# Kernel optimization log

Hardware: AMD Instinct MI355X
Metric: run time of the kernel (lower is better)

The kernel has to match this reference:

```python
import jax, jax.numpy as jnp
import numpy as np

H = 16  # num_heads

def setup_inputs() -> dict:
    key = jax.random.key(0)
    k1, k2, k3, k4 = jax.random.split(key, 4)
    B, N, E = 2, 2048, 2048
    return {
        "hidden_states": jax.random.normal(k1, (B, N, E), jnp.float32),
        "w_fused": jax.random.normal(k2, (E, 3 * E), jnp.float32) * (E ** -0.5),
        "w_proj": jax.random.normal(k3, (E, E), jnp.float32) * (E ** -0.5),
        "b_proj": jax.random.normal(k4, (E,), jnp.float32),
    }

def reference(hidden_states, w_fused, w_proj, b_proj):
    B, N, E = hidden_states.shape
    D = E // H  # head_dim
    qkv = hidden_states @ w_fused                      # [B,N,3E]
    q, k, v = jnp.split(qkv, 3, axis=-1)               # each [B,N,E]
    def to_heads(t):
        return t.reshape(B, N, H, D).transpose(0, 2, 1, 3)  # [B,H,N,D]
    q, k, v = to_heads(q), to_heads(k), to_heads(v)
    scores = jnp.einsum('bhnd,bhmd->bhnm', q, k) / jnp.asarray(D ** 0.5, q.dtype)
    causal = jnp.tril(jnp.ones((N, N), dtype=bool))    # [N,N]
    mask_value = jnp.asarray(jnp.finfo(scores.dtype).min, scores.dtype)
    scores = jnp.where(causal[None, None], scores, mask_value)
    attn_weights = jax.nn.softmax(scores, axis=-1)     # [B,H,N,N]
    attn_out = jnp.einsum('bhnm,bhmd->bhnd', attn_weights, v)
    attn_out = attn_out.transpose(0, 2, 1, 3).reshape(B, N, E)  # b n (h d)
    out = attn_out @ w_proj + b_proj
    return out, attn_weights
```

## Files before the change

### kernel.cpp

```cpp
#include <hip/hip_runtime.h>
#include <hip/hip_bf16.h>

typedef __attribute__((ext_vector_type(4))) float f32x4;
typedef __attribute__((ext_vector_type(8))) __bf16 bf16x8;


__device__ inline unsigned short f2bf(float f) {
  union { float f; unsigned u; } x; x.f = f;
  unsigned r = x.u + 0x7fffu + ((x.u >> 16) & 1u);
  return (unsigned short)(r >> 16);
}

__device__ inline void stage_bf16_tile(const ushort* __restrict__ g, int ldg, ushort* l) {
  int tid = threadIdx.x;
#pragma unroll
  for (int t = 0; t < 4; ++t) {
    int c = tid + t * 256;
    int m = c >> 3, kc = (c & 7) << 3;
    *(int4*)(l + m * 72 + kc) = *(const int4*)(g + (size_t)m * ldg + kc);
  }
}

__device__ inline void mma_tile(const ushort* lA, const ushort* lB, f32x4 acc[4][4]) {
  int lane = threadIdx.x & 63, w = threadIdx.x >> 6;
  int wm = (w & 1) << 6, wn = (w >> 1) << 6;
  int row = lane & 15, quad = lane >> 4;
#pragma unroll
  for (int kk = 0; kk < 64; kk += 32) {
    bf16x8 a[4], b[4];
#pragma unroll
    for (int i = 0; i < 4; ++i)
      a[i] = *(const bf16x8*)(lA + (wm + i * 16 + row) * 72 + kk + quad * 8);
#pragma unroll
    for (int j = 0; j < 4; ++j)
      b[j] = *(const bf16x8*)(lB + (wn + j * 16 + row) * 72 + kk + quad * 8);
#pragma unroll
    for (int i = 0; i < 4; ++i)
#pragma unroll
      for (int j = 0; j < 4; ++j)
        acc[i][j] = __builtin_amdgcn_mfma_f32_16x16x32_bf16(a[i], b[j], acc[i][j], 0, 0, 0);
  }
}

__device__ inline void mma_pv(const ushort* lP, const ushort* lV, int kk2, f32x4 acc[4][4]) {
  int lane = threadIdx.x & 63, w = threadIdx.x >> 6;
  int wm = (w & 1) << 6, wn = (w >> 1) << 6;
  int row = lane & 15, quad = lane >> 4;
#pragma unroll
  for (int kk = 0; kk < 64; kk += 32) {
    bf16x8 a[4], b[4];
#pragma unroll
    for (int i = 0; i < 4; ++i)
      a[i] = *(const bf16x8*)(lP + (wm + i * 16 + row) * 136 + kk2 * 64 + kk + quad * 8);
#pragma unroll
    for (int j = 0; j < 4; ++j)
      b[j] = *(const bf16x8*)(lV + (wn + j * 16 + row) * 72 + kk + quad * 8);
#pragma unroll
    for (int i = 0; i < 4; ++i)
#pragma unroll
      for (int j = 0; j < 4; ++j)
        acc[i][j] = __builtin_amdgcn_mfma_f32_16x16x32_bf16(a[i], b[j], acc[i][j], 0, 0, 0);
  }
}


__global__ __launch_bounds__(256) void k_cvt_bf16(const float* __restrict__ in,
                                                  ushort* __restrict__ out, int n4) {
  int i = blockIdx.x * 256 + threadIdx.x;
  if (i >= n4) return;
  float4 v = *(const float4*)(in + (size_t)i * 4);
  ushort4 o; o.x = f2bf(v.x); o.y = f2bf(v.y); o.z = f2bf(v.z); o.w = f2bf(v.w);
  *(ushort4*)(out + (size_t)i * 4) = o;
}

__global__ __launch_bounds__(256) void k_transpose_bf16(const float* __restrict__ in,
                                                        ushort* __restrict__ out, int R, int C) {
  __shared__ __align__(16) ushort t[64][72];
  int c0 = blockIdx.x << 6, r0 = blockIdx.y << 6;
  int tid = threadIdx.x;
#pragma unroll
  for (int it = 0; it < 4; ++it) {
    int idx = tid + it * 256;
    int r = idx >> 4, c4 = (idx & 15) << 2;
    float4 v = *(const float4*)(in + (size_t)(r0 + r) * C + c0 + c4);
    t[c4][r] = f2bf(v.x); t[c4 + 1][r] = f2bf(v.y);
    t[c4 + 2][r] = f2bf(v.z); t[c4 + 3][r] = f2bf(v.w);
  }
  __syncthreads();
#pragma unroll
  for (int it = 0; it < 4; ++it) {
    int idx = tid + it * 256;
    int c = idx >> 4, r4 = (idx & 15) << 2;
    ushort4 o; o.x = t[c][r4]; o.y = t[c][r4 + 1]; o.z = t[c][r4 + 2]; o.w = t[c][r4 + 3];
    *(ushort4*)(out + (size_t)(c0 + c) * R + r0 + r4) = o;
  }
}

__global__ __launch_bounds__(256) void k_qkv(const ushort* __restrict__ A,
                                             const ushort* __restrict__ Bt,
                                             ushort* __restrict__ qh,
                                             ushort* __restrict__ kh,
                                             ushort* __restrict__ vt) {
  __shared__ __align__(16) ushort lA[128 * 72];
  __shared__ __align__(16) ushort lB[128 * 72];
  int rt = blockIdx.x, ct = blockIdx.y;
  f32x4 z = {0.f, 0.f, 0.f, 0.f};
  f32x4 acc[4][4];
#pragma unroll
  for (int i = 0; i < 4; ++i)
#pragma unroll
    for (int j = 0; j < 4; ++j) acc[i][j] = z;
  for (int kt = 0; kt < 2048; kt += 64) {
    __syncthreads();
    stage_bf16_tile(A + (size_t)rt * 128 * 2048 + kt, 2048, lA);
    stage_bf16_tile(Bt + (size_t)ct * 128 * 2048 + kt, 2048, lB);
    __syncthreads();
    mma_tile(lA, lB, acc);
  }
  int lane = threadIdx.x & 63, w = threadIdx.x >> 6;
  int wm = (w & 1) << 6, wn = (w >> 1) << 6;
  int col = lane & 15, rb = (lane >> 4) << 2;
#pragma unroll
  for (int i = 0; i < 4; ++i)
#pragma unroll
    for (int j = 0; j < 4; ++j)
#pragma unroll
      for (int r = 0; r < 4; ++r) {
        int R = rt * 128 + wm + i * 16 + rb + r;
        int C = ct * 128 + wn + j * 16 + col;
        int b = R >> 11, n = R & 2047;
        int seg = C >> 11, hh = (C >> 7) & 15, d = C & 127;
        int bh = b * 16 + hh;
        float v = acc[i][j][r];
        if (seg == 0)      qh[((size_t)bh * 2048 + n) * 128 + d] = f2bf(v * 0.08838834764831845f);
        else if (seg == 1) kh[((size_t)bh * 2048 + n) * 128 + d] = f2bf(v);
        else               vt[((size_t)bh * 128 + d) * 2048 + n] = f2bf(v);
      }
}

__global__ __launch_bounds__(256, 2) void k_attn(const ushort* __restrict__ qh,
                                                 const ushort* __restrict__ kh,
                                                 const ushort* __restrict__ vt,
                                                 float* __restrict__ attnw,
                                                 ushort* __restrict__ Ao) {
  __shared__ __align__(16) ushort lAB[2 * 128 * 72];
  __shared__ __align__(16) ushort lV[128 * 72];
  __shared__ float mArr[128], lArr[128], invA[128], tm0[128], tm1[128];

  int id = blockIdx.x;
  int r5 = id & 31, p = r5 >> 1;
  int rt = (r5 & 1) ? p : 15 - p;
  int bh = ((id >> 5) << 1) | ((id >> 4) & 1);

  ushort* lA = lAB;
  ushort* lB = lAB + 128 * 72;
  int tid = threadIdx.x;
  int lane = tid & 63, w = tid >> 6;
  int wm = (w & 1) << 6, wn = (w >> 1) << 6;
  int c16 = lane & 15, quad = lane >> 4;

  const ushort* Qb = qh + ((size_t)bh * 2048 + rt * 128) * 128;
  const ushort* Kb = kh + (size_t)bh * 2048 * 128;
  const ushort* Vb = vt + (size_t)bh * 128 * 2048;
  float* Pg = attnw + (size_t)bh * 2048 * 2048 + (size_t)rt * 128 * 2048;

  if (tid < 128) { mArr[tid] = -INFINITY; lArr[tid] = 0.f; }
  __syncthreads();

  f32x4 z = {0.f, 0.f, 0.f, 0.f};
  float* tmw = (wn == 0) ? tm0 : tm1;

  for (int ct = 0; ct <= rt; ++ct) {
    f32x4 acc[4][4];
#pragma unroll
    for (int i = 0; i < 4; ++i)
#pragma unroll
      for (int j = 0; j < 4; ++j) acc[i][j] = z;
#pragma unroll
    for (int kt = 0; kt < 128; kt += 64) {
      __syncthreads();
      stage_bf16_tile(Qb + kt, 128, lA);
      stage_bf16_tile(Kb + (size_t)ct * 128 * 128 + kt, 128, lB);
      __syncthreads();
      mma_tile(lA, lB, acc);
    }
    bool diag = (ct == rt);
#pragma unroll
    for (int i = 0; i < 4; ++i)
#pragma unroll
      for (int r = 0; r < 4; ++r) {
        int lr = wm + i * 16 + quad * 4 + r;
        float mx = -INFINITY;
#pragma unroll
        for (int j = 0; j < 4; ++j) {
          int lc = wn + j * 16 + c16;
          if (!diag || lc <= lr) mx = fmaxf(mx, acc[i][j][r]);
        }
#pragma unroll
        for (int o = 1; o < 16; o <<= 1) mx = fmaxf(mx, __shfl_xor(mx, o));
        if (c16 == 0) tmw[lr] = mx;
      }
    __syncthreads();
    if (tid < 128) {
      float tmax = fmaxf(tm0[tid], tm1[tid]);
      float mo = mArr[tid];
      float mn = fmaxf(mo, tmax);
      float corr = (mo == -INFINITY) ? 0.f : __expf(mo - mn);
      mArr[tid] = mn;
      lArr[tid] *= corr;
    }
    __syncthreads();
#pragma unroll
    for (int i = 0; i < 4; ++i)
#pragma unroll
      for (int r = 0; r < 4; ++r) {
        int lr = wm + i * 16 + quad * 4 + r;
        float mn = mArr[lr];
        float s = 0.f;
#pragma unroll
        for (int j = 0; j < 4; ++j) {
          int lc = wn + j * 16 + c16;
          if (!diag || lc <= lr) s += __expf(acc[i][j][r] - mn);
        }
#pragma unroll
        for (int o = 1; o < 16; o <<= 1) s += __shfl_xor(s, o);
        if (c16 == 0) tmw[lr] = s;
      }
    __syncthreads();
    if (tid < 128) lArr[tid] += tm0[tid] + tm1[tid];
  }
  __syncthreads();
  if (tid < 128) invA[tid] = 1.f / lArr[tid];
  __syncthreads();

  f32x4 o2[4][4];
#pragma unroll
  for (int i = 0; i < 4; ++i)
#pragma unroll
    for (int j = 0; j < 4; ++j) o2[i][j] = z;

  for (int ct = 0; ct <= rt; ++ct) {
    f32x4 acc[4][4];
#pragma unroll
    for (int i = 0; i < 4; ++i)
#pragma unroll
      for (int j = 0; j < 4; ++j) acc[i][j] = z;
#pragma unroll
    for (int kt = 0; kt < 128; kt += 64) {
      __syncthreads();
      stage_bf16_tile(Qb + kt, 128, lA);
      stage_bf16_tile(Kb + (size_t)ct * 128 * 128 + kt, 128, lB);
      __syncthreads();
      mma_tile(lA, lB, acc);
    }
    __syncthreads();
    bool diag = (ct == rt);
    ushort* lP = lAB;
#pragma unroll
    for (int i = 0; i < 4; ++i)
#pragma unroll
      for (int r = 0; r < 4; ++r) {
        int lr = wm + i * 16 + quad * 4 + r;
        float mn = mArr[lr], inv = invA[lr];
        float* prow = Pg + (size_t)lr * 2048 + ct * 128;
#pragma unroll
        for (int j = 0; j < 4; ++j) {
          int lc = wn + j * 16 + c16;
          float e = (!diag || lc <= lr) ? __expf(acc[i][j][r] - mn) * inv : 0.f;
          lP[lr * 136 + lc] = f2bf(e);
          prow[lc] = e;
        }
      }
    stage_bf16_tile(Vb + ct * 128, 2048, lV);
    __syncthreads();
    mma_pv(lP, lV, 0, o2);
    __syncthreads();
    stage_bf16_tile(Vb + ct * 128 + 64, 2048, lV);
    __syncthreads();
    mma_pv(lP, lV, 1, o2);
  }

  float4 z4 = make_float4(0.f, 0.f, 0.f, 0.f);
  for (int ct = rt + 1; ct < 16; ++ct) {
    float* T = Pg + ct * 128;
#pragma unroll
    for (int it = 0; it < 16; ++it) {
      int idx = tid + it * 256;
      int rr = idx >> 5, cc = (idx & 31) << 2;
      *(float4*)(T + (size_t)rr * 2048 + cc) = z4;
    }
  }

  int b = bh >> 4, hh = bh & 15;
#pragma unroll
  for (int i = 0; i < 4; ++i)
#pragma unroll
    for (int j = 0; j < 4; ++j)
#pragma unroll
      for (int r = 0; r < 4; ++r) {
        int R = rt * 128 + wm + i * 16 + quad * 4 + r;
        int C = wn + j * 16 + c16;
        Ao[((size_t)b * 2048 + R) * 2048 + hh * 128 + C] = f2bf(o2[i][j][r]);
      }
}

__global__ __launch_bounds__(256) void k_proj(const ushort* __restrict__ Ao,
                                              const ushort* __restrict__ Wt,
                                              const float* __restrict__ bias,
                                              float* __restrict__ out) {
  int rt = blockIdx.x, ct = blockIdx.y;
  __shared__ __align__(16) ushort lA[128 * 72];
  __shared__ __align__(16) ushort lB[128 * 72];
  f32x4 z = {0.f, 0.f, 0.f, 0.f};
  f32x4 acc[4][4];
#pragma unroll
  for (int i = 0; i < 4; ++i)
#pragma unroll
    for (int j = 0; j < 4; ++j) acc[i][j] = z;
  for (int kt = 0; kt < 2048; kt += 64) {
    __syncthreads();
    stage_bf16_tile(Ao + (size_t)rt * 128 * 2048 + kt, 2048, lA);
    stage_bf16_tile(Wt + (size_t)ct * 128 * 2048 + kt, 2048, lB);
    __syncthreads();
    mma_tile(lA, lB, acc);
  }
  int lane = threadIdx.x & 63, w = threadIdx.x >> 6;
  int wm = (w & 1) << 6, wn = (w >> 1) << 6;
  int col = lane & 15, rb = (lane >> 4) << 2;
#pragma unroll
  for (int i = 0; i < 4; ++i)
#pragma unroll
    for (int j = 0; j < 4; ++j)
#pragma unroll
      for (int r = 0; r < 4; ++r) {
        int R = rt * 128 + wm + i * 16 + rb + r;
        int C = ct * 128 + wn + j * 16 + col;
        out[(size_t)R * 2048 + C] = acc[i][j][r] + bias[C];
      }
}


extern "C" void kernel_launch(void* const* d_in, const int* in_sizes, int n_in,
                              void* d_out, int out_size, void* d_ws, size_t ws_size,
                              hipStream_t stream) {
  const float* hs = (const float*)d_in[0];
  const float* wf = (const float*)d_in[1];
  const float* wp = (const float*)d_in[2];
  const float* bp = (const float*)d_in[3];
  float* out = (float*)d_out;
  float* attnw = out + (size_t)8388608;

  ushort* Hb  = (ushort*)d_ws;
  ushort* Wft = Hb  + (size_t)8388608;
  ushort* Wpt = Wft + (size_t)12582912;
  ushort* qh  = Wpt + (size_t)4194304;
  ushort* kh  = qh  + (size_t)8388608;
  ushort* vt  = kh  + (size_t)8388608;
  ushort* Ao  = vt  + (size_t)8388608;

  k_cvt_bf16<<<8192, 256, 0, stream>>>(hs, Hb, 2097152);
  k_transpose_bf16<<<dim3(96, 32), 256, 0, stream>>>(wf, Wft, 2048, 6144);
  k_transpose_bf16<<<dim3(32, 32), 256, 0, stream>>>(wp, Wpt, 2048, 2048);
  k_qkv<<<dim3(32, 48), 256, 0, stream>>>(Hb, Wft, qh, kh, vt);
  k_attn<<<512, 256, 0, stream>>>(qh, kh, vt, attnw, Ao);
  k_proj<<<dim3(32, 16), 256, 0, stream>>>(Ao, Wpt, bp, out);
}
```

Baseline: 1.129 ms.

## Single-pass online-softmax attention with direct-to-LDS loads and fixup kernel for weights

Attention moves from a two-pass scheme (one pass for max/sum, a second that recomputes QK and does PV) to a single online-softmax pass. Raw scores are written to the attention-weights buffer and later normalised by a separate fixup kernel that also writes the causal zeros. Q is kept in registers, and K/V tiles are staged through XOR-swizzled LDS using global_load_lds. The same swizzled direct-to-LDS staging replaces padded shared tiles in the QKV and projection GEMMs, and attention blocks are remapped for locality. The cost is an extra read and write pass over the large attention-weights tensor in exchange for dropping the QK recompute and part of the LDS traffic.

```diff
diff --git a/kernel.cpp b/kernel.cpp
--- a/kernel.cpp
+++ b/kernel.cpp
@@ -11,50 +11,47 @@
   return (unsigned short)(r >> 16);
 }
 
-__device__ inline void stage_bf16_tile(const ushort* __restrict__ g, int ldg, ushort* l) {
+__device__ inline void gload16(const ushort* g, ushort* l) {
+  __builtin_amdgcn_global_load_lds(
+      (const __attribute__((address_space(1))) unsigned int*)(const void*)g,
+      (__attribute__((address_space(3))) unsigned int*)(void*)l, 16, 0, 0);
+}
+
+__device__ inline void stage64(const ushort* __restrict__ g, int ldg, ushort* l) {
   int tid = threadIdx.x;
 #pragma unroll
   for (int t = 0; t < 4; ++t) {
     int c = tid + t * 256;
-    int m = c >> 3, kc = (c & 7) << 3;
-    *(int4*)(l + m * 72 + kc) = *(const int4*)(g + (size_t)m * ldg + kc);
-  }
-}
-
-__device__ inline void mma_tile(const ushort* lA, const ushort* lB, f32x4 acc[4][4]) {
+    int m = c >> 3, q = (c & 7) ^ (m & 7);
+    gload16(g + (size_t)m * ldg + q * 8, l + c * 8);
+  }
+}
+
+__device__ inline void stage128(const ushort* __restrict__ g, int ldg, ushort* l) {
+  int tid = threadIdx.x;
+#pragma unroll
+  for (int t = 0; t < 8; ++t) {
+    int c = tid + t * 256;
+    int m = c >> 4, q = (c & 15) ^ (m & 15);
+    gload16(g + (size_t)m * ldg + q * 8, l + c * 8);
+  }
+}
+
+__device__ inline void mma_tile64(const ushort* lA, const ushort* lB, f32x4 acc[4][4]) {
   int lane = threadIdx.x & 63, w = threadIdx.x >> 6;
   int wm = (w & 1) << 6, wn = (w >> 1) << 6;
   int row = lane & 15, quad = lane >> 4;
+  int r7 = row & 7;
 #pragma unroll
   for (int kk = 0; kk < 64; kk += 32) {
+    int sw = (((kk >> 3) + quad) ^ r7) << 3;
     bf16x8 a[4], b[4];
 #pragma unroll
     for (int i = 0; i < 4; ++i)
-      a[i] = *(const bf16x8*)(lA + (wm + i * 16 + row) * 72 + kk + quad * 8);
+      a[i] = *(const bf16x8*)(lA + (wm + i * 16 + row) * 64 + sw);
 #pragma unroll
     for (int j = 0; j < 4; ++j)
-      b[j] = *(const bf16x8*)(lB + (wn + j * 16 + row) * 72 + kk + quad * 8);
-#pragma unroll
-    for (int i = 0; i < 4; ++i)
-#pragma unroll
-      for (int j = 0; j < 4; ++j)
-        acc[i][j] = __builtin_amdgcn_mfma_f32_16x16x32_bf16(a[i], b[j], acc[i][j], 0, 0, 0);
-  }
-}
-
-__device__ inline void mma_pv(const ushort* lP, const ushort* lV, int kk2, f32x4 acc[4][4]) {
-  int lane = threadIdx.x & 63, w = threadIdx.x >> 6;
-  int wm = (w & 1) << 6, wn = (w >> 1) << 6;
-  int row = lane & 15, quad = lane >> 4;
-#pragma unroll
-  for (int kk = 0; kk < 64; kk += 32) {
-    bf16x8 a[4], b[4];
-#pragma unroll
-    for (int i = 0; i < 4; ++i)
-      a[i] = *(const bf16x8*)(lP + (wm + i * 16 + row) * 136 + kk2 * 64 + kk + quad * 8);
-#pragma unroll
-    for (int j = 0; j < 4; ++j)
-      b[j] = *(const bf16x8*)(lV + (wn + j * 16 + row) * 72 + kk + quad * 8);
+      b[j] = *(const bf16x8*)(lB + (wn + j * 16 + row) * 64 + sw);
 #pragma unroll
     for (int i = 0; i < 4; ++i)
 #pragma unroll
@@ -101,8 +98,8 @@
                                              ushort* __restrict__ qh,
                                              ushort* __restrict__ kh,
                                              ushort* __restrict__ vt) {
-  __shared__ __align__(16) ushort lA[128 * 72];
-  __shared__ __align__(16) ushort lB[128 * 72];
+  __shared__ __align__(16) ushort lA[128 * 64];
+  __shared__ __align__(16) ushort lB[128 * 64];
   int rt = blockIdx.x, ct = blockIdx.y;
   f32x4 z = {0.f, 0.f, 0.f, 0.f};
   f32x4 acc[4][4];
@@ -112,10 +109,10 @@
     for (int j = 0; j < 4; ++j) acc[i][j] = z;
   for (int kt = 0; kt < 2048; kt += 64) {
     __syncthreads();
-    stage_bf16_tile(A + (size_t)rt * 128 * 2048 + kt, 2048, lA);
-    stage_bf16_tile(Bt + (size_t)ct * 128 * 2048 + kt, 2048, lB);
-    __syncthreads();
-    mma_tile(lA, lB, acc);
+    stage64(A + (size_t)rt * 128 * 2048 + kt, 2048, lA);
+    stage64(Bt + (size_t)ct * 128 * 2048 + kt, 2048, lB);
+    __syncthreads();
+    mma_tile64(lA, lB, acc);
   }
   int lane = threadIdx.x & 63, w = threadIdx.x >> 6;
   int wm = (w & 1) << 6, wn = (w >> 1) << 6;
@@ -142,18 +139,19 @@
                                                  const ushort* __restrict__ kh,
                                                  const ushort* __restrict__ vt,
                                                  float* __restrict__ attnw,
-                                                 ushort* __restrict__ Ao) {
-  __shared__ __align__(16) ushort lAB[2 * 128 * 72];
-  __shared__ __align__(16) ushort lV[128 * 72];
-  __shared__ float mArr[128], lArr[128], invA[128], tm0[128], tm1[128];
-
-  int id = blockIdx.x;
+                                                 ushort* __restrict__ Ao,
+                                                 float* __restrict__ mf,
+                                                 float* __restrict__ il) {
+  __shared__ __align__(16) ushort lKP[128 * 128];
+  __shared__ __align__(16) ushort lV[128 * 128];
+  __shared__ float mArr[128], lArr[128], corrArr[128], invA[128], tm0[128], tm1[128];
+
+  int raw = blockIdx.x;
+  int id = (raw & 7) * 64 + (raw >> 3);
   int r5 = id & 31, p = r5 >> 1;
   int rt = (r5 & 1) ? p : 15 - p;
   int bh = ((id >> 5) << 1) | ((id >> 4) & 1);
 
-  ushort* lA = lAB;
-  ushort* lB = lAB + 128 * 72;
   int tid = threadIdx.x;
   int lane = tid & 63, w = tid >> 6;
   int wm = (w & 1) << 6, wn = (w >> 1) << 6;
@@ -164,26 +162,48 @@
   const ushort* Vb = vt + (size_t)bh * 128 * 2048;
   float* Pg = attnw + (size_t)bh * 2048 * 2048 + (size_t)rt * 128 * 2048;
 
+  bf16x8 q[4][4];
+#pragma unroll
+  for (int i = 0; i < 4; ++i)
+#pragma unroll
+    for (int ks = 0; ks < 4; ++ks)
+      q[i][ks] = *(const bf16x8*)(Qb + (size_t)(wm + i * 16 + c16) * 128 + ks * 32 + quad * 8);
+
   if (tid < 128) { mArr[tid] = -INFINITY; lArr[tid] = 0.f; }
-  __syncthreads();
 
   f32x4 z = {0.f, 0.f, 0.f, 0.f};
+  f32x4 o2[4][4];
+#pragma unroll
+  for (int i = 0; i < 4; ++i)
+#pragma unroll
+    for (int j = 0; j < 4; ++j) o2[i][j] = z;
   float* tmw = (wn == 0) ? tm0 : tm1;
 
   for (int ct = 0; ct <= rt; ++ct) {
+    __syncthreads();
+    stage128(Kb + (size_t)ct * 128 * 128, 128, lKP);
+    __syncthreads();
+    stage128(Vb + ct * 128, 2048, lV);
+
     f32x4 acc[4][4];
 #pragma unroll
     for (int i = 0; i < 4; ++i)
 #pragma unroll
       for (int j = 0; j < 4; ++j) acc[i][j] = z;
 #pragma unroll
-    for (int kt = 0; kt < 128; kt += 64) {
-      __syncthreads();
-      stage_bf16_tile(Qb + kt, 128, lA);
-      stage_bf16_tile(Kb + (size_t)ct * 128 * 128 + kt, 128, lB);
-      __syncthreads();
-      mma_tile(lA, lB, acc);
+    for (int ks = 0; ks < 4; ++ks) {
+      int sw = (((ks << 2) + quad) ^ c16) << 3;
+      bf16x8 b[4];
+#pragma unroll
+      for (int j = 0; j < 4; ++j)
+        b[j] = *(const bf16x8*)(lKP + (wn + j * 16 + c16) * 128 + sw);
+#pragma unroll
+      for (int i = 0; i < 4; ++i)
+#pragma unroll
+        for (int j = 0; j < 4; ++j)
+          acc[i][j] = __builtin_amdgcn_mfma_f32_16x16x32_bf16(q[i][ks], b[j], acc[i][j], 0, 0, 0);
     }
+
     bool diag = (ct == rt);
 #pragma unroll
     for (int i = 0; i < 4; ++i)
@@ -206,21 +226,27 @@
       float mo = mArr[tid];
       float mn = fmaxf(mo, tmax);
       float corr = (mo == -INFINITY) ? 0.f : __expf(mo - mn);
-      mArr[tid] = mn;
-      lArr[tid] *= corr;
+      mArr[tid] = mn; corrArr[tid] = corr; lArr[tid] *= corr;
     }
     __syncthreads();
+
 #pragma unroll
     for (int i = 0; i < 4; ++i)
 #pragma unroll
       for (int r = 0; r < 4; ++r) {
         int lr = wm + i * 16 + quad * 4 + r;
-        float mn = mArr[lr];
+        float mn = mArr[lr], corr = corrArr[lr];
         float s = 0.f;
+        float* prow = Pg + (size_t)lr * 2048 + ct * 128;
 #pragma unroll
         for (int j = 0; j < 4; ++j) {
           int lc = wn + j * 16 + c16;
-          if (!diag || lc <= lr) s += __expf(acc[i][j][r] - mn);
+          float sv = acc[i][j][r];
+          prow[lc] = sv;
+          float e = (!diag || lc <= lr) ? __expf(sv - mn) : 0.f;
+          s += e;
+          lKP[lr * 128 + ((((lc >> 3) ^ (lr & 15)) << 3) | (lc & 7))] = f2bf(e);
+          o2[i][j][r] *= corr;
         }
 #pragma unroll
         for (int o = 1; o < 16; o <<= 1) s += __shfl_xor(s, o);
@@ -228,80 +254,73 @@
       }
     __syncthreads();
     if (tid < 128) lArr[tid] += tm0[tid] + tm1[tid];
+
+#pragma unroll
+    for (int ks = 0; ks < 4; ++ks) {
+      int sw = (((ks << 2) + quad) ^ c16) << 3;
+      bf16x8 a[4], b[4];
+#pragma unroll
+      for (int i = 0; i < 4; ++i)
+        a[i] = *(const bf16x8*)(lKP + (wm + i * 16 + c16) * 128 + sw);
+#pragma unroll
+      for (int j = 0; j < 4; ++j)
+        b[j] = *(const bf16x8*)(lV + (wn + j * 16 + c16) * 128 + sw);
+#pragma unroll
+      for (int i = 0; i < 4; ++i)
+#pragma unroll
+        for (int j = 0; j < 4; ++j)
+          o2[i][j] = __builtin_amdgcn_mfma_f32_16x16x32_bf16(a[i], b[j], o2[i][j], 0, 0, 0);
+    }
+  }
+
+  if (tid < 128) {
+    float iv = 1.f / lArr[tid];
+    invA[tid] = iv;
+    int g = bh * 2048 + rt * 128 + tid;
+    mf[g] = mArr[tid]; il[g] = iv;
   }
   __syncthreads();
-  if (tid < 128) invA[tid] = 1.f / lArr[tid];
-  __syncthreads();
-
-  f32x4 o2[4][4];
-#pragma unroll
-  for (int i = 0; i < 4; ++i)
-#pragma unroll
-    for (int j = 0; j < 4; ++j) o2[i][j] = z;
-
-  for (int ct = 0; ct <= rt; ++ct) {
-    f32x4 acc[4][4];
-#pragma unroll
-    for (int i = 0; i < 4; ++i)
-#pragma unroll
-      for (int j = 0; j < 4; ++j) acc[i][j] = z;
-#pragma unroll
-    for (int kt = 0; kt < 128; kt += 64) {
-      __syncthreads();
-      stage_bf16_tile(Qb + kt, 128, lA);
-      stage_bf16_tile(Kb + (size_t)ct * 128 * 128 + kt, 128, lB);
-      __syncthreads();
-      mma_tile(lA, lB, acc);
+  int b = bh >> 4, hh = bh & 15;
+#pragma unroll
+  for (int i = 0; i < 4; ++i)
+#pragma unroll
+    for (int j = 0; j < 4; ++j)
+#pragma unroll
+      for (int r = 0; r < 4; ++r) {
+        int lr = wm + i * 16 + quad * 4 + r;
+        int R = rt * 128 + lr;
+        int C = wn + j * 16 + c16;
+        Ao[((size_t)b * 2048 + R) * 2048 + hh * 128 + C] = f2bf(o2[i][j][r] * invA[lr]);
+      }
+}
+
+__global__ __launch_bounds__(256) void k_fixup(float* __restrict__ attnw,
+                                               const float* __restrict__ mf,
+                                               const float* __restrict__ il) {
+  int n = blockIdx.x, bh = blockIdx.y;
+  float m = mf[bh * 2048 + n];
+  float inv = il[bh * 2048 + n];
+  float* row = attnw + ((size_t)bh * 2048 + n) * 2048;
+  int tid = threadIdx.x;
+#pragma unroll
+  for (int t = 0; t < 2; ++t) {
+    int c0 = (tid + t * 256) << 2;
+    float4 o;
+    if (c0 + 3 <= n) {
+      float4 s = *(const float4*)(row + c0);
+      o.x = __expf(s.x - m) * inv; o.y = __expf(s.y - m) * inv;
+      o.z = __expf(s.z - m) * inv; o.w = __expf(s.w - m) * inv;
+    } else if (c0 > n) {
+      o = make_float4(0.f, 0.f, 0.f, 0.f);
+    } else {
+      float4 s = *(const float4*)(row + c0);
+      o.x = (c0     <= n) ? __expf(s.x - m) * inv : 0.f;
+      o.y = (c0 + 1 <= n) ? __expf(s.y - m) * inv : 0.f;
+      o.z = (c0 + 2 <= n) ? __expf(s.z - m) * inv : 0.f;
+      o.w = (c0 + 3 <= n) ? __expf(s.w - m) * inv : 0.f;
     }
-    __syncthreads();
-    bool diag = (ct == rt);
-    ushort* lP = lAB;
-#pragma unroll
-    for (int i = 0; i < 4; ++i)
-#pragma unroll
-      for (int r = 0; r < 4; ++r) {
-        int lr = wm + i * 16 + quad * 4 + r;
-        float mn = mArr[lr], inv = invA[lr];
-        float* prow = Pg + (size_t)lr * 2048 + ct * 128;
-#pragma unroll
-        for (int j = 0; j < 4; ++j) {
-          int lc = wn + j * 16 + c16;
-          float e = (!diag || lc <= lr) ? __expf(acc[i][j][r] - mn) * inv : 0.f;
-          lP[lr * 136 + lc] = f2bf(e);
-          prow[lc] = e;
-        }
-      }
-    stage_bf16_tile(Vb + ct * 128, 2048, lV);
-    __syncthreads();
-    mma_pv(lP, lV, 0, o2);
-    __syncthreads();
-    stage_bf16_tile(Vb + ct * 128 + 64, 2048, lV);
-    __syncthreads();
-    mma_pv(lP, lV, 1, o2);
-  }
-
-  float4 z4 = make_float4(0.f, 0.f, 0.f, 0.f);
-  for (int ct = rt + 1; ct < 16; ++ct) {
-    float* T = Pg + ct * 128;
-#pragma unroll
-    for (int it = 0; it < 16; ++it) {
-      int idx = tid + it * 256;
-      int rr = idx >> 5, cc = (idx & 31) << 2;
-      *(float4*)(T + (size_t)rr * 2048 + cc) = z4;
-    }
-  }
-
-  int b = bh >> 4, hh = bh & 15;
-#pragma unroll
-  for (int i = 0; i < 4; ++i)
-#pragma unroll
-    for (int j = 0; j < 4; ++j)
-#pragma unroll
-      for (int r = 0; r < 4; ++r) {
-        int R = rt * 128 + wm + i * 16 + quad * 4 + r;
-        int C = wn + j * 16 + c16;
-        Ao[((size_t)b * 2048 + R) * 2048 + hh * 128 + C] = f2bf(o2[i][j][r]);
-      }
+    *(float4*)(row + c0) = o;
+  }
 }
 
 __global__ __launch_bounds__(256) void k_proj(const ushort* __restrict__ Ao,
@@ -309,8 +328,8 @@
                                               const float* __restrict__ bias,
                                               float* __restrict__ out) {
   int rt = blockIdx.x, ct = blockIdx.y;
-  __shared__ __align__(16) ushort lA[128 * 72];
-  __shared__ __align__(16) ushort lB[128 * 72];
+  __shared__ __align__(16) ushort lA[128 * 64];
+  __shared__ __align__(16) ushort lB[128 * 64];
   f32x4 z = {0.f, 0.f, 0.f, 0.f};
   f32x4 acc[4][4];
 #pragma unroll
@@ -319,10 +338,10 @@
     for (int j = 0; j < 4; ++j) acc[i][j] = z;
   for (int kt = 0; kt < 2048; kt += 64) {
     __syncthreads();
-    stage_bf16_tile(Ao + (size_t)rt * 128 * 2048 + kt, 2048, lA);
-    stage_bf16_tile(Wt + (size_t)ct * 128 * 2048 + kt, 2048, lB);
-    __syncthreads();
-    mma_tile(lA, lB, acc);
+    stage64(Ao + (size_t)rt * 128 * 2048 + kt, 2048, lA);
+    stage64(Wt + (size_t)ct * 128 * 2048 + kt, 2048, lB);
+    __syncthreads();
+    mma_tile64(lA, lB, acc);
   }
   int lane = threadIdx.x & 63, w = threadIdx.x >> 6;
   int wm = (w & 1) << 6, wn = (w >> 1) << 6;
@@ -357,11 +376,14 @@
   ushort* kh  = qh  + (size_t)8388608;
   ushort* vt  = kh  + (size_t)8388608;
   ushort* Ao  = vt  + (size_t)8388608;
+  float* mf = (float*)Hb;
+  float* il = mf + 65536;
 
   k_cvt_bf16<<<8192, 256, 0, stream>>>(hs, Hb, 2097152);
   k_transpose_bf16<<<dim3(96, 32), 256, 0, stream>>>(wf, Wft, 2048, 6144);
   k_transpose_bf16<<<dim3(32, 32), 256, 0, stream>>>(wp, Wpt, 2048, 2048);
   k_qkv<<<dim3(32, 48), 256, 0, stream>>>(Hb, Wft, qh, kh, vt);
-  k_attn<<<512, 256, 0, stream>>>(qh, kh, vt, attnw, Ao);
+  k_attn<<<512, 256, 0, stream>>>(qh, kh, vt, attnw, Ao, mf, il);
+  k_fixup<<<dim3(2048, 32), 256, 0, stream>>>(attnw, mf, il);
   k_proj<<<dim3(32, 16), 256, 0, stream>>>(Ao, Wpt, bp, out);
 }
```

After: 1.451 ms. +28.4%, slower.
